# Optimization experiments

Measured on AMD Instinct MI355X. Metric: run time of the kernel, lower is better.

Reference implementation:

```python
import jax, jax.numpy as jnp
import numpy as np

HID = 64
IN_FEAT = 4 * 3 * 3  # 36
OUT_FEAT = 4
T = 131072


def setup_inputs() -> dict:
    key = jax.random.key(0)
    ks = jax.random.split(key, 16)
    s_in = 1.0 / np.sqrt(IN_FEAT)
    s_h = 1.0 / np.sqrt(HID)
    inp = {
        'obsseq': jax.random.normal(ks[0], (T, 4, 3, 3), dtype=jnp.float32),
        'W1': jax.random.normal(ks[1], (IN_FEAT, HID), dtype=jnp.float32) * s_in,
        'b1': jnp.zeros((HID,), dtype=jnp.float32),
        # GRU input projections (with bias, as in flax GRUCell)
        'Wir': jax.random.normal(ks[2], (HID, HID), dtype=jnp.float32) * s_h,
        'bir': jnp.zeros((HID,), dtype=jnp.float32),
        'Wiz': jax.random.normal(ks[3], (HID, HID), dtype=jnp.float32) * s_h,
        'biz': jnp.zeros((HID,), dtype=jnp.float32),
        'Win': jax.random.normal(ks[4], (HID, HID), dtype=jnp.float32) * s_h,
        'bin': jnp.zeros((HID,), dtype=jnp.float32),
        # GRU hidden projections (hr/hz no bias, hn has bias, as in flax GRUCell)
        'Whr': jax.random.normal(ks[5], (HID, HID), dtype=jnp.float32) * s_h,
        'Whz': jax.random.normal(ks[6], (HID, HID), dtype=jnp.float32) * s_h,
        'Whn': jax.random.normal(ks[7], (HID, HID), dtype=jnp.float32) * s_h,
        'bhn': jnp.zeros((HID,), dtype=jnp.float32),
        'Wend': jax.random.normal(ks[8], (HID, OUT_FEAT), dtype=jnp.float32) * s_h,
        'bend': jnp.zeros((OUT_FEAT,), dtype=jnp.float32),
    }
    return inp


PERM = np.array([1, 0, 3, 2])


def reference(obsseq, W1, b1, Wir, bir, Wiz, biz, Win, bin, Whr, Whz, Whn, bhn, Wend, bend):
    Tn = obsseq.shape[0]
    xs = obsseq.reshape(Tn, -1)                      # [T, 36]
    hs_in = jax.nn.relu(xs @ W1 + b1)                # [T, 64]
    # Precompute all input-side gate projections (parallel over T)
    xr = hs_in @ Wir + bir                           # [T, 64]
    xz = hs_in @ Wiz + biz
    xn = hs_in @ Win + bin

    def step(h, inp):
        xr_t, xz_t, xn_t = inp
        r = jax.nn.sigmoid(xr_t + h @ Whr)
        z = jax.nn.sigmoid(xz_t + h @ Whz)
        n = jnp.tanh(xn_t + r * (h @ Whn + bhn))
        h_new = (1.0 - z) * n + z * h
        return h_new, h_new

    h0 = jnp.zeros((HID,), dtype=hs_in.dtype)
    _, hs_out = jax.lax.scan(step, h0, (xr, xz, xn))  # [T, 64]
    zs = hs_out @ Wend + bend                         # [T, 4]
    return zs[:, PERM]
```

## Files before the change

kernel.cpp:

```cpp
#include <hip/hip_runtime.h>
#include <cstddef>

#define T_LEN 131072
#define CH 16
#define CHUNK_T 128
#define NBLK (T_LEN / CHUNK_T)
#define WARMUP 64

typedef float float4_t __attribute__((ext_vector_type(4)));

__device__ __forceinline__ float fast_sigmoid(float x) {
  float e = __builtin_amdgcn_exp2f(x * -1.44269504088896340736f);
  return __builtin_amdgcn_rcpf(1.0f + e);
}

__device__ __forceinline__ float fast_tanh(float x) {
  float e = __builtin_amdgcn_exp2f(x * 2.88539008177792681472f);
  return 1.0f - 2.0f * __builtin_amdgcn_rcpf(1.0f + e);
}

__global__ __launch_bounds__(256, 4) void prep2_kernel(
    const float* __restrict__ obs, const float* __restrict__ W1,
    const float* __restrict__ b1,
    const float* __restrict__ Wir, const float* __restrict__ bir,
    const float* __restrict__ Wiz, const float* __restrict__ biz,
    const float* __restrict__ Win, const float* __restrict__ bin,
    float* __restrict__ gates)
{
  __shared__ float wbuf[4096];
  __shared__ float hbuf[64 * 64];
  __shared__ float sb1[64];
  __shared__ float sbg[192];

  const int tid = threadIdx.x;
  const int tt  = tid >> 2;
  const int q   = tid & 3;
  const int t   = blockIdx.x * 64 + tt;

  for (int i = tid; i < 2304; i += 256) wbuf[i] = W1[i];
  if (tid < 64) {
    sb1[tid] = b1[tid];
    sbg[tid] = bir[tid];
    sbg[64 + tid] = biz[tid];
    sbg[128 + tid] = bin[tid];
  }
  __syncthreads();

  {
    float4_t x4[9];
    const float4_t* op = (const float4_t*)(obs + (size_t)t * 36);
#pragma unroll
    for (int c = 0; c < 9; c++) x4[c] = op[c];

    float4_t h4[4];
    {
      const float4_t* bv = (const float4_t*)(sb1 + q * 16);
#pragma unroll
      for (int k = 0; k < 4; k++) h4[k] = bv[k];
    }
#pragma unroll
    for (int c = 0; c < 9; c++) {
#pragma unroll
      for (int e = 0; e < 4; e++) {
        const float xv = x4[c][e];
        const float4_t* wrow = (const float4_t*)(wbuf + (c * 4 + e) * 64 + q * 16);
#pragma unroll
        for (int k = 0; k < 4; k++) h4[k] += xv * wrow[k];
      }
    }
    float4_t* hdst = (float4_t*)(hbuf + tt * 64 + q * 16);
#pragma unroll
    for (int k = 0; k < 4; k++) {
      float4_t v = h4[k];
      v.x = fmaxf(v.x, 0.0f); v.y = fmaxf(v.y, 0.0f);
      v.z = fmaxf(v.z, 0.0f); v.w = fmaxf(v.w, 0.0f);
      hdst[k] = v;
    }
  }
  __syncthreads();

  for (int g = 0; g < 3; g++) {
    const float* wsrc = (g == 0) ? Wir : (g == 1) ? Wiz : Win;
    for (int i = tid; i < 4096; i += 256) wbuf[i] = wsrc[i];
    __syncthreads();

    float4_t acc[4];
    {
      const float4_t* bv = (const float4_t*)(sbg + g * 64 + q * 16);
#pragma unroll
      for (int k = 0; k < 4; k++) acc[k] = bv[k];
    }
    const float4_t* hrow = (const float4_t*)(hbuf + tt * 64);
    for (int kk = 0; kk < 16; kk++) {
      const float4_t hv = hrow[kk];
#pragma unroll
      for (int e = 0; e < 4; e++) {
        const float h = hv[e];
        const float4_t* wrow = (const float4_t*)(wbuf + (kk * 4 + e) * 64 + q * 16);
#pragma unroll
        for (int k = 0; k < 4; k++) acc[k] += h * wrow[k];
      }
    }
    float4_t* gout = (float4_t*)(gates + (size_t)t * 192 + g * 64 + q * 16);
#pragma unroll
    for (int k = 0; k < 4; k++) gout[k] = acc[k];
    __syncthreads();
  }
}

#define REP16(X) X(0) X(1) X(2) X(3) X(4) X(5) X(6) X(7) \
                 X(8) X(9) X(10) X(11) X(12) X(13) X(14) X(15)

#define DECLW(c) float wr##c, wz##c, wn##c;
#define INITW_R(c) wr##c = gstage[(kbase + (c)) * 64 + j];
#define INITW_Z(c) wz##c = gstage[(kbase + (c)) * 64 + j];
#define INITW_N(c) wn##c = gstage[(kbase + (c)) * 64 + j];
#define PINW(c) asm volatile("" : "+v"(wr##c), "+v"(wz##c), "+v"(wn##c));

#define DECLH(c) float hh##c = 0.0f;
#define RL(c) hh##c = __builtin_bit_cast(float, \
    __builtin_amdgcn_readlane(__builtin_bit_cast(int, hn), (c)));

#define FMA2(ce, co) \
  sR0 = __builtin_fmaf(wr##ce, hh##ce, sR0); sR1 = __builtin_fmaf(wr##co, hh##co, sR1); \
  sZ0 = __builtin_fmaf(wz##ce, hh##ce, sZ0); sZ1 = __builtin_fmaf(wz##co, hh##co, sZ1); \
  sN0 = __builtin_fmaf(wn##ce, hh##ce, sN0); sN1 = __builtin_fmaf(wn##co, hh##co, sN1);

#define LDS_BARRIER() asm volatile("s_waitcnt lgkmcnt(0)\n\ts_barrier")

#define STEP(s) { \
  const float xr = gcur[(s)*192 + jr]; \
  const float xz = gcur[(s)*192 + 64 + jr]; \
  const float xn = gcur[(s)*192 + 128 + jr]; \
  float sR0 = 0.f, sR1 = 0.f, sZ0 = 0.f, sZ1 = 0.f, sN0 = 0.f, sN1 = 0.f; \
  FMA2(0,1) FMA2(2,3) FMA2(4,5) FMA2(6,7) \
  FMA2(8,9) FMA2(10,11) FMA2(12,13) FMA2(14,15) \
  partf4[((s)&1)*256 + wslot + j] = float4_t{sR0 + sR1, sZ0 + sZ1, sN0 + sN1, 0.0f}; \
  LDS_BARRIER(); \
  const float4_t q0 = partf4[((s)&1)*256 +       jr]; \
  const float4_t q1 = partf4[((s)&1)*256 +  64 + jr]; \
  const float4_t q2 = partf4[((s)&1)*256 + 128 + jr]; \
  const float4_t q3 = partf4[((s)&1)*256 + 192 + jr]; \
  const float r = fast_sigmoid(xr + ((q0.x + q1.x) + (q2.x + q3.x))); \
  const float z = fast_sigmoid(xz + ((q0.y + q1.y) + (q2.y + q3.y))); \
  const float n = fast_tanh(xn + r * (((q0.z + q1.z) + (q2.z + q3.z)) + bh)); \
  const float hn = n + z * (hprev - n);       \
  hprev = hn; \
  REP16(RL)                                   \
  if (lane16) hstage[(s)*64 + jr] = hn;       \
}

__global__ __launch_bounds__(256, 4) void scan_chunk_kernel(
    const float* __restrict__ gates,
    const float* __restrict__ Whr, const float* __restrict__ Whz,
    const float* __restrict__ Whn, const float* __restrict__ bhn,
    const float* __restrict__ Wend, const float* __restrict__ bend,
    float* __restrict__ out)
{
  __shared__ float gstage[2 * CH * 192];
  __shared__ float4_t partf4[512];
  __shared__ float hstage[CH * 64];
  __shared__ float sWendT[4 * 64];
  __shared__ float sbend[4];
  const int tid = threadIdx.x;
  const int j = tid & 63;
  const int wid = tid >> 6;
  const int kbase = wid * 16;
  const int wslot = wid * 64;
  const int l15 = j & 15;
  const int jr = kbase + l15;
  const bool lane16 = (j < 16);

  REP16(DECLW)
  for (int i = tid; i < 4096; i += 256) gstage[i] = Whr[i];
  __syncthreads();
  REP16(INITW_R)
  __syncthreads();
  for (int i = tid; i < 4096; i += 256) gstage[i] = Whz[i];
  __syncthreads();
  REP16(INITW_Z)
  __syncthreads();
  for (int i = tid; i < 4096; i += 256) gstage[i] = Whn[i];
  __syncthreads();
  REP16(INITW_N)
  {
    const int k = tid >> 2, o = tid & 3;
    sWendT[o * 64 + k] = Wend[k * 4 + (o ^ 1)];
    if (tid < 4) sbend[tid] = bend[tid ^ 1];
  }
  REP16(PINW)
  float bh = bhn[jr];
  asm volatile("" : "+v"(bh));

  REP16(DECLH)
  float hprev = 0.0f;

  const int b = blockIdx.x;
  const int wu = (b == 0) ? 0 : WARMUP;
  const int wskip = wu / CH;
  const int nch = wskip + CHUNK_T / CH;
  const float* gbase = gates + (size_t)(b * CHUNK_T - wu) * 192;

  __syncthreads();

  {
    const float4_t* gsrc = (const float4_t*)gbase;
    const float4_t a = gsrc[tid], bb = gsrc[256 + tid], cc = gsrc[512 + tid];
    float4_t* gdst = (float4_t*)gstage;
    gdst[tid] = a; gdst[256 + tid] = bb; gdst[512 + tid] = cc;
  }
  LDS_BARRIER();

  for (int c = 0; c < nch; c++) {
    const float4_t* gsrc = (const float4_t*)(gbase + (size_t)(c + 1) * (CH * 192));
    const float4_t ga = gsrc[tid], gb = gsrc[256 + tid], gc = gsrc[512 + tid];

    const float* gcur = gstage + (c & 1) * (CH * 192);
    STEP(0)  STEP(1)  STEP(2)  STEP(3)
    STEP(4)  STEP(5)  STEP(6)  STEP(7)
    STEP(8)  STEP(9)  STEP(10) STEP(11)
    STEP(12) STEP(13) STEP(14) STEP(15)

    LDS_BARRIER();
    {
      float4_t* gdst = (float4_t*)(gstage + ((c + 1) & 1) * (CH * 192));
      gdst[tid] = ga; gdst[256 + tid] = gb; gdst[512 + tid] = gc;
      if (c >= wskip) {
        const int tt = tid >> 4;
        const int o  = (tid >> 2) & 3;
        const int kq = tid & 3;
        const float4_t* h4 = (const float4_t*)(hstage + tt * 64 + kq * 16);
        const float4_t* w4 = (const float4_t*)(sWendT + o * 64 + kq * 16);
        float acc = 0.0f;
#pragma unroll
        for (int i = 0; i < 4; i++) {
          const float4_t hv = h4[i], wv = w4[i];
          acc += hv.x * wv.x + hv.y * wv.y + hv.z * wv.z + hv.w * wv.w;
        }
        acc += __shfl_xor(acc, 1);
        acc += __shfl_xor(acc, 2);
        if (kq == 0) {
          const int gt = b * CHUNK_T + (c - wskip) * CH + tt;
          out[gt * 4 + o] = acc + sbend[o];
        }
      }
    }
    LDS_BARRIER();
  }
}

extern "C" void kernel_launch(void* const* d_in, const int* in_sizes, int n_in,
                              void* d_out, int out_size, void* d_ws, size_t ws_size,
                              hipStream_t stream) {
  (void)in_sizes; (void)n_in; (void)out_size; (void)ws_size;
  const float* obs  = (const float*)d_in[0];
  const float* W1   = (const float*)d_in[1];
  const float* b1   = (const float*)d_in[2];
  const float* Wir  = (const float*)d_in[3];
  const float* bir  = (const float*)d_in[4];
  const float* Wiz  = (const float*)d_in[5];
  const float* biz  = (const float*)d_in[6];
  const float* Win  = (const float*)d_in[7];
  const float* bin  = (const float*)d_in[8];
  const float* Whr  = (const float*)d_in[9];
  const float* Whz  = (const float*)d_in[10];
  const float* Whn  = (const float*)d_in[11];
  const float* bhn  = (const float*)d_in[12];
  const float* Wend = (const float*)d_in[13];
  const float* bend = (const float*)d_in[14];
  float* out = (float*)d_out;

  float* gates = (float*)d_ws;

  prep2_kernel<<<T_LEN / 64, 256, 0, stream>>>(obs, W1, b1, Wir, bir, Wiz, biz,
                                               Win, bin, gates);
  scan_chunk_kernel<<<NBLK, 256, 0, stream>>>(gates, Whr, Whz, Whn, bhn,
                                              Wend, bend, out);
}
```

Measured before the change: 322.0 us.

## Restructure gate precompute kernel to register-resident weights with per-step cross-wave reduction

Replaces the LDS-tiled input projection kernel with one that keeps W1 and the three input gate weight slices in registers. It iterates over 128 timesteps per block, broadcasting the hidden features via readlane and reducing partial sums through LDS with a barrier each step. This removes repeated LDS weight reads but serializes timesteps within a block and adds a barrier per step, with only a quarter of lanes storing results.

```diff
diff --git a/kernel.cpp b/kernel.cpp
--- a/kernel.cpp
+++ b/kernel.cpp
@@ -6,6 +6,7 @@
 #define CHUNK_T 128
 #define NBLK (T_LEN / CHUNK_T)
 #define WARMUP 64
+#define PTB 128
 
 typedef float float4_t __attribute__((ext_vector_type(4)));
 
@@ -19,7 +20,34 @@
   return 1.0f - 2.0f * __builtin_amdgcn_rcpf(1.0f + e);
 }
 
-__global__ __launch_bounds__(256, 4) void prep2_kernel(
+#define REP16(X) X(0) X(1) X(2) X(3) X(4) X(5) X(6) X(7) \
+                 X(8) X(9) X(10) X(11) X(12) X(13) X(14) X(15)
+
+#define DECLW(c) float wr##c, wz##c, wn##c;
+#define INITW_R(c) wr##c = wstage[(kbase + (c)) * 64 + j];
+#define INITW_Z(c) wz##c = wstage[(kbase + (c)) * 64 + j];
+#define INITW_N(c) wn##c = wstage[(kbase + (c)) * 64 + j];
+#define PINW(c) asm volatile("" : "+v"(wr##c), "+v"(wz##c), "+v"(wn##c));
+
+#define FMA2(ce, co) \
+  sR0 = __builtin_fmaf(wr##ce, hh##ce, sR0); sR1 = __builtin_fmaf(wr##co, hh##co, sR1); \
+  sZ0 = __builtin_fmaf(wz##ce, hh##ce, sZ0); sZ1 = __builtin_fmaf(wz##co, hh##co, sZ1); \
+  sN0 = __builtin_fmaf(wn##ce, hh##ce, sN0); sN1 = __builtin_fmaf(wn##co, hh##co, sN1);
+
+#define LDS_BARRIER() asm volatile("s_waitcnt lgkmcnt(0)\n\ts_barrier")
+
+#define DECLW1(c) float w1_##c;
+#define INITW1(c) w1_##c = wstage[(c) * 64 + jr];
+#define PINW1(c) asm volatile("" : "+v"(w1_##c));
+#define REP36(X) X(0) X(1) X(2) X(3) X(4) X(5) X(6) X(7) X(8) \
+                 X(9) X(10) X(11) X(12) X(13) X(14) X(15) X(16) X(17) \
+                 X(18) X(19) X(20) X(21) X(22) X(23) X(24) X(25) X(26) \
+                 X(27) X(28) X(29) X(30) X(31) X(32) X(33) X(34) X(35)
+
+#define RLH(c) const float hh##c = __builtin_bit_cast(float, \
+    __builtin_amdgcn_readlane(__builtin_bit_cast(int, h1), (c)));
+
+__global__ __launch_bounds__(256, 4) void prep4_kernel(
     const float* __restrict__ obs, const float* __restrict__ W1,
     const float* __restrict__ b1,
     const float* __restrict__ Wir, const float* __restrict__ bir,
@@ -27,106 +55,82 @@
     const float* __restrict__ Win, const float* __restrict__ bin,
     float* __restrict__ gates)
 {
-  __shared__ float wbuf[4096];
-  __shared__ float hbuf[64 * 64];
-  __shared__ float sb1[64];
-  __shared__ float sbg[192];
+  __shared__ float wstage[4096];
+  __shared__ float4_t partf4[512];
 
   const int tid = threadIdx.x;
-  const int tt  = tid >> 2;
-  const int q   = tid & 3;
-  const int t   = blockIdx.x * 64 + tt;
-
-  for (int i = tid; i < 2304; i += 256) wbuf[i] = W1[i];
-  if (tid < 64) {
-    sb1[tid] = b1[tid];
-    sbg[tid] = bir[tid];
-    sbg[64 + tid] = biz[tid];
-    sbg[128 + tid] = bin[tid];
-  }
-  __syncthreads();
-
-  {
-    float4_t x4[9];
-    const float4_t* op = (const float4_t*)(obs + (size_t)t * 36);
-#pragma unroll
-    for (int c = 0; c < 9; c++) x4[c] = op[c];
-
-    float4_t h4[4];
-    {
-      const float4_t* bv = (const float4_t*)(sb1 + q * 16);
-#pragma unroll
-      for (int k = 0; k < 4; k++) h4[k] = bv[k];
+  const int j = tid & 63;
+  const int wid = tid >> 6;
+  const int kbase = wid * 16;
+  const int wslot = wid * 64;
+  const int jr = kbase + (j & 15);
+  const bool lane16 = (j < 16);
+
+  REP16(DECLW)
+  for (int i = tid; i < 4096; i += 256) wstage[i] = Wir[i];
+  __syncthreads();
+  REP16(INITW_R)
+  __syncthreads();
+  for (int i = tid; i < 4096; i += 256) wstage[i] = Wiz[i];
+  __syncthreads();
+  REP16(INITW_Z)
+  __syncthreads();
+  for (int i = tid; i < 4096; i += 256) wstage[i] = Win[i];
+  __syncthreads();
+  REP16(INITW_N)
+  __syncthreads();
+  REP36(DECLW1)
+  for (int i = tid; i < 2304; i += 256) wstage[i] = W1[i];
+  __syncthreads();
+  REP36(INITW1)
+  REP16(PINW)
+  REP36(PINW1)
+
+  float b1v = b1[jr];
+  float bR = bir[jr], bZ = biz[jr], bN = bin[jr];
+  asm volatile("" : "+v"(b1v), "+v"(bR), "+v"(bZ), "+v"(bN));
+
+  const int t0 = blockIdx.x * PTB;
+
+#define H1F(c, acc) acc = __builtin_fmaf(xrow[c], w1_##c, acc);
+  for (int tt = 0; tt < PTB; ++tt) {
+    const int t = t0 + tt;
+    const float* __restrict__ xrow = obs + (size_t)t * 36;
+    float a0 = b1v, a1 = 0.f, a2 = 0.f, a3 = 0.f;
+    H1F(0,a0) H1F(1,a1) H1F(2,a2) H1F(3,a3)
+    H1F(4,a0) H1F(5,a1) H1F(6,a2) H1F(7,a3)
+    H1F(8,a0) H1F(9,a1) H1F(10,a2) H1F(11,a3)
+    H1F(12,a0) H1F(13,a1) H1F(14,a2) H1F(15,a3)
+    H1F(16,a0) H1F(17,a1) H1F(18,a2) H1F(19,a3)
+    H1F(20,a0) H1F(21,a1) H1F(22,a2) H1F(23,a3)
+    H1F(24,a0) H1F(25,a1) H1F(26,a2) H1F(27,a3)
+    H1F(28,a0) H1F(29,a1) H1F(30,a2) H1F(31,a3)
+    H1F(32,a0) H1F(33,a1) H1F(34,a2) H1F(35,a3)
+    const float h1 = fmaxf((a0 + a1) + (a2 + a3), 0.0f);
+    REP16(RLH)
+    float sR0 = 0.f, sR1 = 0.f, sZ0 = 0.f, sZ1 = 0.f, sN0 = 0.f, sN1 = 0.f;
+    FMA2(0,1) FMA2(2,3) FMA2(4,5) FMA2(6,7)
+    FMA2(8,9) FMA2(10,11) FMA2(12,13) FMA2(14,15)
+    partf4[(tt & 1) * 256 + wslot + j] = float4_t{sR0 + sR1, sZ0 + sZ1, sN0 + sN1, 0.0f};
+    LDS_BARRIER();
+    const float4_t q0 = partf4[(tt & 1) * 256 +       jr];
+    const float4_t q1 = partf4[(tt & 1) * 256 +  64 + jr];
+    const float4_t q2 = partf4[(tt & 1) * 256 + 128 + jr];
+    const float4_t q3 = partf4[(tt & 1) * 256 + 192 + jr];
+    const float gr = bR + ((q0.x + q1.x) + (q2.x + q3.x));
+    const float gz = bZ + ((q0.y + q1.y) + (q2.y + q3.y));
+    const float gn = bN + ((q0.z + q1.z) + (q2.z + q3.z));
+    if (lane16) {
+      float* gp = gates + (size_t)t * 192;
+      gp[jr] = gr; gp[64 + jr] = gz; gp[128 + jr] = gn;
     }
-#pragma unroll
-    for (int c = 0; c < 9; c++) {
-#pragma unroll
-      for (int e = 0; e < 4; e++) {
-        const float xv = x4[c][e];
-        const float4_t* wrow = (const float4_t*)(wbuf + (c * 4 + e) * 64 + q * 16);
-#pragma unroll
-        for (int k = 0; k < 4; k++) h4[k] += xv * wrow[k];
-      }
-    }
-    float4_t* hdst = (float4_t*)(hbuf + tt * 64 + q * 16);
-#pragma unroll
-    for (int k = 0; k < 4; k++) {
-      float4_t v = h4[k];
-      v.x = fmaxf(v.x, 0.0f); v.y = fmaxf(v.y, 0.0f);
-      v.z = fmaxf(v.z, 0.0f); v.w = fmaxf(v.w, 0.0f);
-      hdst[k] = v;
-    }
-  }
-  __syncthreads();
-
-  for (int g = 0; g < 3; g++) {
-    const float* wsrc = (g == 0) ? Wir : (g == 1) ? Wiz : Win;
-    for (int i = tid; i < 4096; i += 256) wbuf[i] = wsrc[i];
-    __syncthreads();
-
-    float4_t acc[4];
-    {
-      const float4_t* bv = (const float4_t*)(sbg + g * 64 + q * 16);
-#pragma unroll
-      for (int k = 0; k < 4; k++) acc[k] = bv[k];
-    }
-    const float4_t* hrow = (const float4_t*)(hbuf + tt * 64);
-    for (int kk = 0; kk < 16; kk++) {
-      const float4_t hv = hrow[kk];
-#pragma unroll
-      for (int e = 0; e < 4; e++) {
-        const float h = hv[e];
-        const float4_t* wrow = (const float4_t*)(wbuf + (kk * 4 + e) * 64 + q * 16);
-#pragma unroll
-        for (int k = 0; k < 4; k++) acc[k] += h * wrow[k];
-      }
-    }
-    float4_t* gout = (float4_t*)(gates + (size_t)t * 192 + g * 64 + q * 16);
-#pragma unroll
-    for (int k = 0; k < 4; k++) gout[k] = acc[k];
-    __syncthreads();
-  }
-}
-
-#define REP16(X) X(0) X(1) X(2) X(3) X(4) X(5) X(6) X(7) \
-                 X(8) X(9) X(10) X(11) X(12) X(13) X(14) X(15)
-
-#define DECLW(c) float wr##c, wz##c, wn##c;
-#define INITW_R(c) wr##c = gstage[(kbase + (c)) * 64 + j];
-#define INITW_Z(c) wz##c = gstage[(kbase + (c)) * 64 + j];
-#define INITW_N(c) wn##c = gstage[(kbase + (c)) * 64 + j];
-#define PINW(c) asm volatile("" : "+v"(wr##c), "+v"(wz##c), "+v"(wn##c));
+  }
+#undef H1F
+}
 
 #define DECLH(c) float hh##c = 0.0f;
 #define RL(c) hh##c = __builtin_bit_cast(float, \
     __builtin_amdgcn_readlane(__builtin_bit_cast(int, hn), (c)));
-
-#define FMA2(ce, co) \
-  sR0 = __builtin_fmaf(wr##ce, hh##ce, sR0); sR1 = __builtin_fmaf(wr##co, hh##co, sR1); \
-  sZ0 = __builtin_fmaf(wz##ce, hh##ce, sZ0); sZ1 = __builtin_fmaf(wz##co, hh##co, sZ1); \
-  sN0 = __builtin_fmaf(wn##ce, hh##ce, sN0); sN1 = __builtin_fmaf(wn##co, hh##co, sN1);
-
-#define LDS_BARRIER() asm volatile("s_waitcnt lgkmcnt(0)\n\ts_barrier")
 
 #define STEP(s) { \
   const float xr = gcur[(s)*192 + jr]; \
@@ -150,6 +154,10 @@
   if (lane16) hstage[(s)*64 + jr] = hn;       \
 }
 
+#define INITWS_R(c) wr##c = gstage[(kbase + (c)) * 64 + j];
+#define INITWS_Z(c) wz##c = gstage[(kbase + (c)) * 64 + j];
+#define INITWS_N(c) wn##c = gstage[(kbase + (c)) * 64 + j];
+
 __global__ __launch_bounds__(256, 4) void scan_chunk_kernel(
     const float* __restrict__ gates,
     const float* __restrict__ Whr, const float* __restrict__ Whz,
@@ -174,15 +182,15 @@
   REP16(DECLW)
   for (int i = tid; i < 4096; i += 256) gstage[i] = Whr[i];
   __syncthreads();
-  REP16(INITW_R)
+  REP16(INITWS_R)
   __syncthreads();
   for (int i = tid; i < 4096; i += 256) gstage[i] = Whz[i];
   __syncthreads();
-  REP16(INITW_Z)
+  REP16(INITWS_Z)
   __syncthreads();
   for (int i = tid; i < 4096; i += 256) gstage[i] = Whn[i];
   __syncthreads();
-  REP16(INITW_N)
+  REP16(INITWS_N)
   {
     const int k = tid >> 2, o = tid & 3;
     sWendT[o * 64 + k] = Wend[k * 4 + (o ^ 1)];
@@ -272,8 +280,8 @@
 
   float* gates = (float*)d_ws;
 
-  prep2_kernel<<<T_LEN / 64, 256, 0, stream>>>(obs, W1, b1, Wir, bir, Wiz, biz,
-                                               Win, bin, gates);
+  prep4_kernel<<<T_LEN / PTB, 256, 0, stream>>>(obs, W1, b1, Wir, bir, Wiz, biz,
+                                                Win, bin, gates);
   scan_chunk_kernel<<<NBLK, 256, 0, stream>>>(gates, Whr, Whz, Whn, bhn,
                                               Wend, bend, out);
 }
```

After: 389.8 us. 21.0% more time.

## Merge prep and scan into one kernel with per-chunk flag synchronization

Applied to the files above, without the earlier changes.

Fuses the gate-projection prep kernel and the chunked GRU scan kernel into a single launch. Blocks are interleaved as two prep blocks per scan block, and each scan block spin-waits on release/acquire flags for the prep blocks covering its range (including warmup). This lets scans start without waiting for the whole prep grid and removes a kernel boundary. It also shortens the warmup from 64 to 48 steps and pads the prep hidden buffer to reduce LDS bank conflicts. The costs are an extra memset launch, spin-waits that can deadlock-guard via a timeout, reliance on dispatch order, and slightly lower accuracy from the shorter warmup.

```diff
diff --git a/kernel.cpp b/kernel.cpp
--- a/kernel.cpp
+++ b/kernel.cpp
@@ -4,8 +4,9 @@
 #define T_LEN 131072
 #define CH 16
 #define CHUNK_T 128
-#define NBLK (T_LEN / CHUNK_T)
-#define WARMUP 64
+#define NSCAN (T_LEN / CHUNK_T)
+#define NPREP (T_LEN / 64)
+#define WARMUP 48
 
 typedef float float4_t __attribute__((ext_vector_type(4)));
 
@@ -19,150 +20,173 @@
   return 1.0f - 2.0f * __builtin_amdgcn_rcpf(1.0f + e);
 }
 
-__global__ __launch_bounds__(256, 4) void prep2_kernel(
+#define REP16(X) X(0) X(1) X(2) X(3) X(4) X(5) X(6) X(7) \
+                 X(8) X(9) X(10) X(11) X(12) X(13) X(14) X(15)
+
+#define LDS_BARRIER() asm volatile("s_waitcnt lgkmcnt(0)\n\ts_barrier")
+
+
+union MergedShared {
+  struct {
+    float wbuf[4096];
+    float hbuf[64 * 68];
+    float sb1[64];
+    float sbg[192];
+  } p;
+  struct {
+    float gstage[2 * CH * 192];
+    float4_t partf4[512];
+    float hstage[CH * 64];
+    float wendT[4 * 64];
+    float sbend[4];
+  } s;
+};
+
+#define DECLW(c) float wr##c, wz##c, wn##c;
+#define INITWS_R(c) wr##c = gstage[(kbase + (c)) * 64 + j];
+#define INITWS_Z(c) wz##c = gstage[(kbase + (c)) * 64 + j];
+#define INITWS_N(c) wn##c = gstage[(kbase + (c)) * 64 + j];
+#define PINW(c) asm volatile("" : "+v"(wr##c), "+v"(wz##c), "+v"(wn##c));
+
+#define DECLH(c) float hh##c = 0.0f;
+#define RL(c) hh##c = __builtin_bit_cast(float, \
+    __builtin_amdgcn_readlane(__builtin_bit_cast(int, hn), (c)));
+
+#define FMA2(ce, co) \
+  sR0 = __builtin_fmaf(wr##ce, hh##ce, sR0); sR1 = __builtin_fmaf(wr##co, hh##co, sR1); \
+  sZ0 = __builtin_fmaf(wz##ce, hh##ce, sZ0); sZ1 = __builtin_fmaf(wz##co, hh##co, sZ1); \
+  sN0 = __builtin_fmaf(wn##ce, hh##ce, sN0); sN1 = __builtin_fmaf(wn##co, hh##co, sN1);
+
+#define STEP(st) { \
+  const float xr = gcur[(st)*192 + jr]; \
+  const float xz = gcur[(st)*192 + 64 + jr]; \
+  const float xn = gcur[(st)*192 + 128 + jr]; \
+  float sR0 = 0.f, sR1 = 0.f, sZ0 = 0.f, sZ1 = 0.f, sN0 = 0.f, sN1 = 0.f; \
+  FMA2(0,1) FMA2(2,3) FMA2(4,5) FMA2(6,7) \
+  FMA2(8,9) FMA2(10,11) FMA2(12,13) FMA2(14,15) \
+  partf4[((st)&1)*256 + wslot + j] = float4_t{sR0 + sR1, sZ0 + sZ1, sN0 + sN1, 0.0f}; \
+  LDS_BARRIER(); \
+  const float4_t q0 = partf4[((st)&1)*256 +       jr]; \
+  const float4_t q1 = partf4[((st)&1)*256 +  64 + jr]; \
+  const float4_t q2 = partf4[((st)&1)*256 + 128 + jr]; \
+  const float4_t q3 = partf4[((st)&1)*256 + 192 + jr]; \
+  const float r = fast_sigmoid(xr + ((q0.x + q1.x) + (q2.x + q3.x))); \
+  const float z = fast_sigmoid(xz + ((q0.y + q1.y) + (q2.y + q3.y))); \
+  const float n = fast_tanh(xn + r * (((q0.z + q1.z) + (q2.z + q3.z)) + bh)); \
+  const float hn = n + z * (hprev - n);       \
+  hprev = hn; \
+  REP16(RL) \
+  if (lane16) hstage[(st)*64 + jr] = hn; \
+}
+
+__global__ __launch_bounds__(256, 4) void merged_kernel(
     const float* __restrict__ obs, const float* __restrict__ W1,
     const float* __restrict__ b1,
     const float* __restrict__ Wir, const float* __restrict__ bir,
     const float* __restrict__ Wiz, const float* __restrict__ biz,
     const float* __restrict__ Win, const float* __restrict__ bin,
-    float* __restrict__ gates)
-{
-  __shared__ float wbuf[4096];
-  __shared__ float hbuf[64 * 64];
-  __shared__ float sb1[64];
-  __shared__ float sbg[192];
-
-  const int tid = threadIdx.x;
-  const int tt  = tid >> 2;
-  const int q   = tid & 3;
-  const int t   = blockIdx.x * 64 + tt;
-
-  for (int i = tid; i < 2304; i += 256) wbuf[i] = W1[i];
-  if (tid < 64) {
-    sb1[tid] = b1[tid];
-    sbg[tid] = bir[tid];
-    sbg[64 + tid] = biz[tid];
-    sbg[128 + tid] = bin[tid];
-  }
-  __syncthreads();
-
-  {
-    float4_t x4[9];
-    const float4_t* op = (const float4_t*)(obs + (size_t)t * 36);
-#pragma unroll
-    for (int c = 0; c < 9; c++) x4[c] = op[c];
-
-    float4_t h4[4];
-    {
-      const float4_t* bv = (const float4_t*)(sb1 + q * 16);
-#pragma unroll
-      for (int k = 0; k < 4; k++) h4[k] = bv[k];
-    }
-#pragma unroll
-    for (int c = 0; c < 9; c++) {
-#pragma unroll
-      for (int e = 0; e < 4; e++) {
-        const float xv = x4[c][e];
-        const float4_t* wrow = (const float4_t*)(wbuf + (c * 4 + e) * 64 + q * 16);
-#pragma unroll
-        for (int k = 0; k < 4; k++) h4[k] += xv * wrow[k];
-      }
-    }
-    float4_t* hdst = (float4_t*)(hbuf + tt * 64 + q * 16);
-#pragma unroll
-    for (int k = 0; k < 4; k++) {
-      float4_t v = h4[k];
-      v.x = fmaxf(v.x, 0.0f); v.y = fmaxf(v.y, 0.0f);
-      v.z = fmaxf(v.z, 0.0f); v.w = fmaxf(v.w, 0.0f);
-      hdst[k] = v;
-    }
-  }
-  __syncthreads();
-
-  for (int g = 0; g < 3; g++) {
-    const float* wsrc = (g == 0) ? Wir : (g == 1) ? Wiz : Win;
-    for (int i = tid; i < 4096; i += 256) wbuf[i] = wsrc[i];
-    __syncthreads();
-
-    float4_t acc[4];
-    {
-      const float4_t* bv = (const float4_t*)(sbg + g * 64 + q * 16);
-#pragma unroll
-      for (int k = 0; k < 4; k++) acc[k] = bv[k];
-    }
-    const float4_t* hrow = (const float4_t*)(hbuf + tt * 64);
-    for (int kk = 0; kk < 16; kk++) {
-      const float4_t hv = hrow[kk];
-#pragma unroll
-      for (int e = 0; e < 4; e++) {
-        const float h = hv[e];
-        const float4_t* wrow = (const float4_t*)(wbuf + (kk * 4 + e) * 64 + q * 16);
-#pragma unroll
-        for (int k = 0; k < 4; k++) acc[k] += h * wrow[k];
-      }
-    }
-    float4_t* gout = (float4_t*)(gates + (size_t)t * 192 + g * 64 + q * 16);
-#pragma unroll
-    for (int k = 0; k < 4; k++) gout[k] = acc[k];
-    __syncthreads();
-  }
-}
-
-#define REP16(X) X(0) X(1) X(2) X(3) X(4) X(5) X(6) X(7) \
-                 X(8) X(9) X(10) X(11) X(12) X(13) X(14) X(15)
-
-#define DECLW(c) float wr##c, wz##c, wn##c;
-#define INITW_R(c) wr##c = gstage[(kbase + (c)) * 64 + j];
-#define INITW_Z(c) wz##c = gstage[(kbase + (c)) * 64 + j];
-#define INITW_N(c) wn##c = gstage[(kbase + (c)) * 64 + j];
-#define PINW(c) asm volatile("" : "+v"(wr##c), "+v"(wz##c), "+v"(wn##c));
-
-#define DECLH(c) float hh##c = 0.0f;
-#define RL(c) hh##c = __builtin_bit_cast(float, \
-    __builtin_amdgcn_readlane(__builtin_bit_cast(int, hn), (c)));
-
-#define FMA2(ce, co) \
-  sR0 = __builtin_fmaf(wr##ce, hh##ce, sR0); sR1 = __builtin_fmaf(wr##co, hh##co, sR1); \
-  sZ0 = __builtin_fmaf(wz##ce, hh##ce, sZ0); sZ1 = __builtin_fmaf(wz##co, hh##co, sZ1); \
-  sN0 = __builtin_fmaf(wn##ce, hh##ce, sN0); sN1 = __builtin_fmaf(wn##co, hh##co, sN1);
-
-#define LDS_BARRIER() asm volatile("s_waitcnt lgkmcnt(0)\n\ts_barrier")
-
-#define STEP(s) { \
-  const float xr = gcur[(s)*192 + jr]; \
-  const float xz = gcur[(s)*192 + 64 + jr]; \
-  const float xn = gcur[(s)*192 + 128 + jr]; \
-  float sR0 = 0.f, sR1 = 0.f, sZ0 = 0.f, sZ1 = 0.f, sN0 = 0.f, sN1 = 0.f; \
-  FMA2(0,1) FMA2(2,3) FMA2(4,5) FMA2(6,7) \
-  FMA2(8,9) FMA2(10,11) FMA2(12,13) FMA2(14,15) \
-  partf4[((s)&1)*256 + wslot + j] = float4_t{sR0 + sR1, sZ0 + sZ1, sN0 + sN1, 0.0f}; \
-  LDS_BARRIER(); \
-  const float4_t q0 = partf4[((s)&1)*256 +       jr]; \
-  const float4_t q1 = partf4[((s)&1)*256 +  64 + jr]; \
-  const float4_t q2 = partf4[((s)&1)*256 + 128 + jr]; \
-  const float4_t q3 = partf4[((s)&1)*256 + 192 + jr]; \
-  const float r = fast_sigmoid(xr + ((q0.x + q1.x) + (q2.x + q3.x))); \
-  const float z = fast_sigmoid(xz + ((q0.y + q1.y) + (q2.y + q3.y))); \
-  const float n = fast_tanh(xn + r * (((q0.z + q1.z) + (q2.z + q3.z)) + bh)); \
-  const float hn = n + z * (hprev - n);       \
-  hprev = hn; \
-  REP16(RL)                                   \
-  if (lane16) hstage[(s)*64 + jr] = hn;       \
-}
-
-__global__ __launch_bounds__(256, 4) void scan_chunk_kernel(
-    const float* __restrict__ gates,
     const float* __restrict__ Whr, const float* __restrict__ Whz,
     const float* __restrict__ Whn, const float* __restrict__ bhn,
     const float* __restrict__ Wend, const float* __restrict__ bend,
+    float* __restrict__ gates, int* __restrict__ flags,
     float* __restrict__ out)
 {
-  __shared__ float gstage[2 * CH * 192];
-  __shared__ float4_t partf4[512];
-  __shared__ float hstage[CH * 64];
-  __shared__ float sWendT[4 * 64];
-  __shared__ float sbend[4];
+  __shared__ MergedShared sh;
   const int tid = threadIdx.x;
+  const int gid = blockIdx.x;
+  const int grp = gid / 3;
+  const int role = gid - grp * 3;
+
+  if (role < 2) {
+    const int p = grp * 2 + role;
+    float* const wbuf = sh.p.wbuf;
+    float* const hbuf = sh.p.hbuf;
+
+    const int tt  = tid >> 2;
+    const int q   = tid & 3;
+    const int t   = p * 64 + tt;
+
+    for (int i = tid; i < 2304; i += 256) wbuf[i] = W1[i];
+    if (tid < 64) {
+      sh.p.sb1[tid] = b1[tid];
+      sh.p.sbg[tid] = bir[tid];
+      sh.p.sbg[64 + tid] = biz[tid];
+      sh.p.sbg[128 + tid] = bin[tid];
+    }
+    __syncthreads();
+
+    {
+      float4_t x4[9];
+      const float4_t* op = (const float4_t*)(obs + (size_t)t * 36);
+#pragma unroll
+      for (int c = 0; c < 9; c++) x4[c] = op[c];
+
+      float4_t h4[4];
+      {
+        const float4_t* bv = (const float4_t*)(sh.p.sb1 + q * 16);
+#pragma unroll
+        for (int k = 0; k < 4; k++) h4[k] = bv[k];
+      }
+#pragma unroll
+      for (int c = 0; c < 9; c++) {
+#pragma unroll
+        for (int e = 0; e < 4; e++) {
+          const float xv = x4[c][e];
+          const float4_t* wrow = (const float4_t*)(wbuf + (c * 4 + e) * 64 + q * 16);
+#pragma unroll
+          for (int k = 0; k < 4; k++) h4[k] += xv * wrow[k];
+        }
+      }
+      float4_t* hdst = (float4_t*)(hbuf + tt * 68 + q * 16);
+#pragma unroll
+      for (int k = 0; k < 4; k++) {
+        float4_t v = h4[k];
+        v.x = fmaxf(v.x, 0.0f); v.y = fmaxf(v.y, 0.0f);
+        v.z = fmaxf(v.z, 0.0f); v.w = fmaxf(v.w, 0.0f);
+        hdst[k] = v;
+      }
+    }
+    __syncthreads();
+
+    for (int gi = 0; gi < 3; gi++) {
+      const float* wsrc = (gi == 0) ? Wir : (gi == 1) ? Wiz : Win;
+      for (int i = tid; i < 4096; i += 256) wbuf[i] = wsrc[i];
+      __syncthreads();
+
+      float4_t acc[4];
+      {
+        const float4_t* bv = (const float4_t*)(sh.p.sbg + gi * 64 + q * 16);
+#pragma unroll
+        for (int k = 0; k < 4; k++) acc[k] = bv[k];
+      }
+      const float4_t* hrow = (const float4_t*)(hbuf + tt * 68);
+      for (int kk = 0; kk < 16; kk++) {
+        const float4_t hv = hrow[kk];
+#pragma unroll
+        for (int e = 0; e < 4; e++) {
+          const float h = hv[e];
+          const float4_t* wrow = (const float4_t*)(wbuf + (kk * 4 + e) * 64 + q * 16);
+#pragma unroll
+          for (int k = 0; k < 4; k++) acc[k] += h * wrow[k];
+        }
+      }
+      float4_t* gout = (float4_t*)(gates + (size_t)t * 192 + gi * 64 + q * 16);
+#pragma unroll
+      for (int k = 0; k < 4; k++) gout[k] = acc[k];
+      __syncthreads();
+    }
+
+    if (tid == 0)
+      __hip_atomic_store(&flags[p], 1, __ATOMIC_RELEASE, __HIP_MEMORY_SCOPE_AGENT);
+    return;
+  }
+
+  const int b = grp;
+  float* const gstage = sh.s.gstage;
+  float4_t* const partf4 = sh.s.partf4;
+  float* const hstage = sh.s.hstage;
+  float* const wendT  = sh.s.wendT;
+
   const int j = tid & 63;
   const int wid = tid >> 6;
   const int kbase = wid * 16;
@@ -174,19 +198,19 @@
   REP16(DECLW)
   for (int i = tid; i < 4096; i += 256) gstage[i] = Whr[i];
   __syncthreads();
-  REP16(INITW_R)
+  REP16(INITWS_R)
   __syncthreads();
   for (int i = tid; i < 4096; i += 256) gstage[i] = Whz[i];
   __syncthreads();
-  REP16(INITW_Z)
+  REP16(INITWS_Z)
   __syncthreads();
   for (int i = tid; i < 4096; i += 256) gstage[i] = Whn[i];
   __syncthreads();
-  REP16(INITW_N)
+  REP16(INITWS_N)
   {
     const int k = tid >> 2, o = tid & 3;
-    sWendT[o * 64 + k] = Wend[k * 4 + (o ^ 1)];
-    if (tid < 4) sbend[tid] = bend[tid ^ 1];
+    wendT[o * 64 + k] = Wend[k * 4 + (o ^ 1)];
+    if (tid < 4) sh.s.sbend[tid] = bend[tid ^ 1];
   }
   REP16(PINW)
   float bh = bhn[jr];
@@ -195,12 +219,23 @@
   REP16(DECLH)
   float hprev = 0.0f;
 
-  const int b = blockIdx.x;
   const int wu = (b == 0) ? 0 : WARMUP;
   const int wskip = wu / CH;
   const int nch = wskip + CHUNK_T / CH;
   const float* gbase = gates + (size_t)(b * CHUNK_T - wu) * 192;
 
+  if (tid == 0) {
+    const int lo = (2 * b - 1 > 0) ? 2 * b - 1 : 0;
+    const int hi = (2 * b + 1 < NPREP - 1) ? 2 * b + 1 : NPREP - 1;
+    const unsigned long long t0 = __builtin_amdgcn_s_memrealtime();
+    for (int f = lo; f <= hi; ++f) {
+      while (__hip_atomic_load(&flags[f], __ATOMIC_ACQUIRE,
+                               __HIP_MEMORY_SCOPE_AGENT) == 0) {
+        __builtin_amdgcn_s_sleep(8);
+        if (__builtin_amdgcn_s_memrealtime() - t0 > 200000000ull) break;
+      }
+    }
+  }
   __syncthreads();
 
   {
@@ -226,11 +261,11 @@
       float4_t* gdst = (float4_t*)(gstage + ((c + 1) & 1) * (CH * 192));
       gdst[tid] = ga; gdst[256 + tid] = gb; gdst[512 + tid] = gc;
       if (c >= wskip) {
-        const int tt = tid >> 4;
-        const int o  = (tid >> 2) & 3;
-        const int kq = tid & 3;
-        const float4_t* h4 = (const float4_t*)(hstage + tt * 64 + kq * 16);
-        const float4_t* w4 = (const float4_t*)(sWendT + o * 64 + kq * 16);
+        const int tt2 = tid >> 4;
+        const int o   = (tid >> 2) & 3;
+        const int kq  = tid & 3;
+        const float4_t* h4 = (const float4_t*)(hstage + tt2 * 64 + kq * 16);
+        const float4_t* w4 = (const float4_t*)(wendT + o * 64 + kq * 16);
         float acc = 0.0f;
 #pragma unroll
         for (int i = 0; i < 4; i++) {
@@ -240,8 +275,8 @@
         acc += __shfl_xor(acc, 1);
         acc += __shfl_xor(acc, 2);
         if (kq == 0) {
-          const int gt = b * CHUNK_T + (c - wskip) * CH + tt;
-          out[gt * 4 + o] = acc + sbend[o];
+          const int gt = b * CHUNK_T + (c - wskip) * CH + tt2;
+          out[(size_t)gt * 4 + o] = acc + sh.s.sbend[o];
         }
       }
     }
@@ -271,9 +306,10 @@
   float* out = (float*)d_out;
 
   float* gates = (float*)d_ws;
-
-  prep2_kernel<<<T_LEN / 64, 256, 0, stream>>>(obs, W1, b1, Wir, bir, Wiz, biz,
-                                               Win, bin, gates);
-  scan_chunk_kernel<<<NBLK, 256, 0, stream>>>(gates, Whr, Whz, Whn, bhn,
-                                              Wend, bend, out);
-}
+  int* flags = (int*)((char*)d_ws + (size_t)T_LEN * 192 * sizeof(float));
+
+  hipMemsetAsync(flags, 0, NPREP * sizeof(int), stream);
+  merged_kernel<<<NPREP + NSCAN, 256, 0, stream>>>(
+      obs, W1, b1, Wir, bir, Wiz, biz, Win, bin,
+      Whr, Whz, Whn, bhn, Wend, bend, gates, flags, out);
+}
```

Measured after the change: 610.4 us. 1.9x slower.
